# Optimization experiments

Measured on AMD Instinct MI355X. Metric: run time of the kernel, lower is better.

## Reference

```python
import jax, jax.numpy as jnp
import numpy as np

SCALE = 0.25
POOL = (7, 7)
SR = 2          # sampling_ratio
EPS = 1e-5      # LayerNorm eps
B, N, C, H, W = 4, 256, 256, 128, 128
D = 1024
IN_DIM = C * POOL[0] * POOL[1]


def _layer_norm(x, g, b):
    m = x.mean(-1, keepdims=True)
    v = ((x - m) ** 2).mean(-1, keepdims=True)
    return (x - m) / jnp.sqrt(v + EPS) * g + b


def _roi_align_one(feat, ys, xs):
    # feat [C,H,W]; ys [N,PH]; xs [N,PW] sample coords in feature-map space
    Cc, Hh, Ww = feat.shape
    y = ys[:, :, None]                      # [N,PH,1]
    x = xs[:, None, :]                      # [N,1,PW]
    valid = (y > -1.0) & (y < Hh) & (x > -1.0) & (x < Ww)  # torchvision semantics
    yc = jnp.clip(y, 0.0, Hh - 1)
    xc = jnp.clip(x, 0.0, Ww - 1)
    y0 = jnp.floor(yc).astype(jnp.int32)
    x0 = jnp.floor(xc).astype(jnp.int32)
    y1 = jnp.minimum(y0 + 1, Hh - 1)
    x1 = jnp.minimum(x0 + 1, Ww - 1)
    ly = yc - y0; lx = xc - x0
    hy = 1.0 - ly; hx = 1.0 - lx
    flat = feat.reshape(Cc, Hh * Ww)
    g = lambda yi, xi: flat[:, yi * Ww + xi]            # [C,N,PH,PW]
    val = (hy * hx) * g(y0, x0) + (hy * lx) * g(y0, x1) \
        + (ly * hx) * g(y1, x0) + (ly * lx) * g(y1, x1)
    return jnp.where(valid, val, 0.0)                    # [C,N,PH,PW]


def roi_align(feats, boxes):
    # feats [B,C,H,W]; boxes [B,N,4] in image coords -> pooled [B,N,C,ph,pw]
    Bb, Cc, Hh, Ww = feats.shape
    ph, pw = POOL
    b = boxes * SCALE
    bx1, by1, bx2, by2 = b[..., 0], b[..., 1], b[..., 2], b[..., 3]
    rw = jnp.maximum(bx2 - bx1, 1.0)
    rh = jnp.maximum(by2 - by1, 1.0)
    bh = rh / ph
    bw = rw / pw
    # sample offset k -> bin k//SR, sub-sample k%SR: (k+0.5)/SR bin-units
    oy = (jnp.arange(ph * SR, dtype=feats.dtype) + 0.5) / SR
    ox = (jnp.arange(pw * SR, dtype=feats.dtype) + 0.5) / SR
    ys = by1[..., None] + bh[..., None] * oy             # [B,N,ph*SR]
    xs = bx1[..., None] + bw[..., None] * ox             # [B,N,pw*SR]
    vals = jax.vmap(_roi_align_one)(feats, ys, xs)       # [B,C,N,PH,PW]
    Nn = boxes.shape[1]
    vals = vals.transpose(0, 2, 1, 3, 4).reshape(Bb, Nn, Cc, ph, SR, pw, SR)
    return vals.mean(axis=(4, 6))                        # avg over 2x2 samples


def setup_inputs() -> dict:
    key = jax.random.key(0)
    ks = jax.random.split(key, 8)
    feats = jax.random.normal(ks[0], (B, C, H, W), dtype=jnp.float32)
    r = jax.random.uniform(ks[1], (B, N, 4), dtype=jnp.float32)
    x1 = r[..., 0] * (512 - 64)
    y1 = r[..., 1] * (512 - 64)
    x2 = x1 + 4.0 + r[..., 2] * 60.0
    y2 = y1 + 4.0 + r[..., 3] * 60.0
    lines_box = jnp.stack([x1, y1, x2, y2], axis=-1)
    img_sizes = jnp.full((B, 2), 512, dtype=jnp.int32)
    W1 = jax.random.normal(ks[2], (IN_DIM, D), dtype=jnp.float32) / np.sqrt(IN_DIM)
    b1 = jnp.zeros((D,), jnp.float32)
    W2 = jax.random.normal(ks[3], (D, D), dtype=jnp.float32) / np.sqrt(D)
    b2 = jnp.zeros((D,), jnp.float32)
    bbox_W = jax.random.normal(ks[4], (4, D), dtype=jnp.float32) / 2.0
    bbox_b = jnp.zeros((D,), jnp.float32)
    ln_bbox_g = jnp.ones((D,), jnp.float32); ln_bbox_b = jnp.zeros((D,), jnp.float32)
    ln_add_g = jnp.ones((D,), jnp.float32); ln_add_b = jnp.zeros((D,), jnp.float32)
    return {"feats": feats, "lines_box": lines_box, "img_sizes": img_sizes,
            "W1": W1, "b1": b1, "W2": W2, "b2": b2,
            "bbox_W": bbox_W, "bbox_b": bbox_b,
            "ln_bbox_g": ln_bbox_g, "ln_bbox_b": ln_bbox_b,
            "ln_add_g": ln_add_g, "ln_add_b": ln_add_b}


def reference(feats, lines_box, img_sizes, W1, b1, W2, b2, bbox_W, bbox_b,
              ln_bbox_g, ln_bbox_b, ln_add_g, ln_add_b):
    Bb = feats.shape[0]
    Hh, Ww = feats.shape[-2:]
    Nn = lines_box.shape[1]
    pooled = roi_align(feats, lines_box).reshape(Bb, Nn, -1)   # [B,N,C*ph*pw]
    h = jax.nn.relu(pooled @ W1 + b1) @ W2 + b2                # [B,N,D]
    # per-image box normalization: x*scale/feats_W, y*scale/feats_H
    norm = SCALE * jnp.array([1.0 / Ww, 1.0 / Hh, 1.0 / Ww, 1.0 / Hh], feats.dtype)
    nb = lines_box * norm
    p = _layer_norm(nb @ bbox_W + bbox_b, ln_bbox_g, ln_bbox_b)
    return _layer_norm(h + p, ln_add_g, ln_add_b)              # [B,N,D]
```

## Files before the change

kernel.cpp:

```cpp
#include <hip/hip_runtime.h>
#include <hip/hip_bf16.h>

typedef __attribute__((ext_vector_type(8))) short short8;
typedef __attribute__((ext_vector_type(4))) float floatx4;

#define AS1(p) ((const __attribute__((address_space(1))) void*)(p))
#define AS3(p) ((__attribute__((address_space(3))) void*)(p))

__device__ __forceinline__ float bf_lo(unsigned u) { return __uint_as_float(u << 16); }
__device__ __forceinline__ float bf_hi(unsigned u) { return __uint_as_float(u & 0xffff0000u); }

__global__ __launch_bounds__(512) void prep_kernel(
    const float* __restrict__ feats, const float* __restrict__ W1, const float* __restrict__ W2,
    __hip_bfloat16* __restrict__ featsT, __hip_bfloat16* __restrict__ W1T,
    __hip_bfloat16* __restrict__ W2T)
{
    __shared__ float tile[256][68];
    const int t = threadIdx.x;
    const int w = t >> 6, l = t & 63;
    const int bid = blockIdx.x;

    const float* src;
    __hip_bfloat16* dst;
    size_t sstride, dstride;

    if (bid < 1024) {
        const int b = bid >> 8, hwt = bid & 255;
        src = feats + (size_t)b * 256 * 16384 + hwt * 64;
        sstride = 16384;
        dst = featsT + ((size_t)b * 16384 + hwt * 64) * 256;
        dstride = 256;
    } else if (bid < 1808) {
        const int r = bid - 1024;
        const int bin = r >> 4, nt = r & 15;
        src = W1 + (size_t)bin * 1024 + nt * 64;
        sstride = 49 * 1024;
        dst = W1T + (size_t)(nt * 64) * 12544 + bin * 256;
        dstride = 12544;
    } else {
        const int r = bid - 1808;
        const int kt = r >> 4, nt = r & 15;
        src = W2 + (size_t)(kt * 256) * 1024 + nt * 64;
        sstride = 1024;
        dst = W2T + (size_t)(nt * 64) * 1024 + kt * 256;
        dstride = 1024;
    }

    #pragma unroll
    for (int i = 0; i < 8; ++i) {
        const int r  = i * 32 + w * 4 + (l >> 4);
        const int c4 = (l & 15) * 4;
        const float4 v = *(const float4*)(src + (size_t)r * sstride + c4);
        *(float4*)&tile[r][c4 ^ (((r >> 3) & 15) << 2)] = v;
    }
    __syncthreads();

    #pragma unroll
    for (int i = 0; i < 4; ++i) {
        const int d  = i * 16 + w * 2 + (l >> 5);
        const int a  = l & 31;
        const int c8 = a * 8;
        const int dsw = d ^ ((a & 15) << 2);
        union { __hip_bfloat16 h[8]; uint4 u; } o;
        #pragma unroll
        for (int j = 0; j < 8; ++j)
            o.h[j] = __float2bfloat16(tile[c8 + j][dsw]);
        *(uint4*)(dst + (size_t)d * dstride + c8) = o.u;
    }
}

__global__ __launch_bounds__(256) void roi_kernel4(
    const __hip_bfloat16* __restrict__ featsT, const float* __restrict__ boxes,
    __hip_bfloat16* __restrict__ pooled)
{
    __shared__ int   sy0[14], sy1[14], sx0[14], sx1[14];
    __shared__ float sly[14], svy[14], slx[14], svx[14];
    const int tid  = threadIdx.x;
    const int bn   = blockIdx.x >> 1;
    const int half = blockIdx.x & 1;
    if (tid < 28) {
        const int  i   = tid % 14;
        const bool isx = tid >= 14;
        const float lo = boxes[bn * 4 + (isx ? 0 : 1)] * 0.25f;
        const float hi = boxes[bn * 4 + (isx ? 2 : 3)] * 0.25f;
        const float szb = fmaxf(hi - lo, 1.0f) * (1.0f / 7.0f);
        const float coord = lo + szb * ((i + 0.5f) * 0.5f);
        const float valid = (coord > -1.0f && coord < 128.0f) ? 1.0f : 0.0f;
        const float cc = fminf(fmaxf(coord, 0.0f), 127.0f);
        const int i0 = (int)floorf(cc);
        const int i1 = min(i0 + 1, 127);
        const float l = cc - (float)i0;
        if (isx) { sx0[i] = i0; sx1[i] = i1; slx[i] = l; svx[i] = valid; }
        else     { sy0[i] = i0; sy1[i] = i1; sly[i] = l; svy[i] = valid; }
    }
    __syncthreads();
    const int wave = tid >> 6;
    const int lane = tid & 63;
    const int sub  = lane >> 5;
    const int co   = lane & 31;
    const int b    = bn >> 8;
    const __hip_bfloat16* fb = featsT + (size_t)b * 4194304 + co * 8;
    __hip_bfloat16* po = pooled + (size_t)bn * 12544 + co * 8;

    const int pstart = (half ? 12 : 0) + wave;
    const int pend   = half ? 25 : 12;
    for (int p = pstart; p < pend; p += 4) {
        int bin = 2 * p + sub;
        if (bin > 48) bin = 48;
        const int ph = (bin * 37) >> 8;
        const int pw = bin - ph * 7;
        float s0 = 0.f, s1 = 0.f, s2 = 0.f, s3 = 0.f;
        float s4 = 0.f, s5 = 0.f, s6 = 0.f, s7 = 0.f;
        #pragma unroll
        for (int sy = 0; sy < 2; ++sy) {
            const int iy = ph * 2 + sy;
            const int y0 = sy0[iy], y1 = sy1[iy];
            const float ly = sly[iy], wy = svy[iy];
            const float hy = 1.f - ly;
            #pragma unroll
            for (int sx = 0; sx < 2; ++sx) {
                const int ix = pw * 2 + sx;
                const int x0 = sx0[ix], x1 = sx1[ix];
                const float lx = slx[ix], wx = svx[ix];
                const float hx = 1.f - lx;
                const uint4 u00 = *(const uint4*)(fb + (((y0 << 7) + x0) * 256));
                const uint4 u01 = *(const uint4*)(fb + (((y0 << 7) + x1) * 256));
                const uint4 u10 = *(const uint4*)(fb + (((y1 << 7) + x0) * 256));
                const uint4 u11 = *(const uint4*)(fb + (((y1 << 7) + x1) * 256));
                const float wv  = wy * wx;
                const float w00 = hy * hx * wv, w01 = hy * lx * wv;
                const float w10 = ly * hx * wv, w11 = ly * lx * wv;
                s0 += w00 * bf_lo(u00.x) + w01 * bf_lo(u01.x) + w10 * bf_lo(u10.x) + w11 * bf_lo(u11.x);
                s1 += w00 * bf_hi(u00.x) + w01 * bf_hi(u01.x) + w10 * bf_hi(u10.x) + w11 * bf_hi(u11.x);
                s2 += w00 * bf_lo(u00.y) + w01 * bf_lo(u01.y) + w10 * bf_lo(u10.y) + w11 * bf_lo(u11.y);
                s3 += w00 * bf_hi(u00.y) + w01 * bf_hi(u01.y) + w10 * bf_hi(u10.y) + w11 * bf_hi(u11.y);
                s4 += w00 * bf_lo(u00.z) + w01 * bf_lo(u01.z) + w10 * bf_lo(u10.z) + w11 * bf_lo(u11.z);
                s5 += w00 * bf_hi(u00.z) + w01 * bf_hi(u01.z) + w10 * bf_hi(u10.z) + w11 * bf_hi(u11.z);
                s6 += w00 * bf_lo(u00.w) + w01 * bf_lo(u01.w) + w10 * bf_lo(u10.w) + w11 * bf_lo(u11.w);
                s7 += w00 * bf_hi(u00.w) + w01 * bf_hi(u01.w) + w10 * bf_hi(u10.w) + w11 * bf_hi(u11.w);
            }
        }
        union { __hip_bfloat16 h[8]; uint4 u; } o;
        o.h[0] = __float2bfloat16(s0 * 0.25f);
        o.h[1] = __float2bfloat16(s1 * 0.25f);
        o.h[2] = __float2bfloat16(s2 * 0.25f);
        o.h[3] = __float2bfloat16(s3 * 0.25f);
        o.h[4] = __float2bfloat16(s4 * 0.25f);
        o.h[5] = __float2bfloat16(s5 * 0.25f);
        o.h[6] = __float2bfloat16(s6 * 0.25f);
        o.h[7] = __float2bfloat16(s7 * 0.25f);
        *(uint4*)(po + bin * 256) = o.u;
    }
}

__global__ __launch_bounds__(512, 2) void gemm1_8phase(
    const __hip_bfloat16* __restrict__ A,
    const __hip_bfloat16* __restrict__ BT,
    __hip_bfloat16* __restrict__ Cpart)
{
    constexpr int K = 12544;
    constexpr int KCHUNK = 896;
    constexpr int NKT = 14;
    constexpr int ITERS = 7;

    __shared__ char lds[131072];

    const int bid = blockIdx.x;
    const int xcd = bid & 7;
    const int sl  = bid >> 3;
    const int z   = xcd + 8 * (sl >> 4);
    if (z >= 14) return;
    const int tile = sl & 15;
    const int by = tile >> 2, bx = tile & 3;
    const int m0 = by << 8, n0 = bx << 8;
    const int k0 = z * KCHUNK;

    const int tid  = threadIdx.x;
    const int lane = tid & 63;
    const int wave = tid >> 6;
    const int wm   = wave >> 2;
    const int wn   = wave & 3;
    const int l15  = lane & 15;
    const int kq   = (lane >> 4) << 3;

    floatx4 acc[8][4] = {};
    short8 bf[4][2];

    auto stage = [&](const __hip_bfloat16* gsrc, int ldsoff) {
        #pragma unroll
        for (int j = 0; j < 2; ++j) {
            const int lin = j * 8192 + tid * 16;
            const int r   = lin >> 7;
            const int cs  = ((lin & 127) ^ ((r & 7) << 4)) >> 1;
            __builtin_amdgcn_global_load_lds(AS1(gsrc + (size_t)r * K + cs),
                                             AS3(lds + ldsoff + lin), 16, 0, 0);
        }
    };

#define PHASE(SLOT, MQ, FIRSTB, STAGE_STMT, VM)                                    \
    {                                                                               \
        if (FIRSTB) {                                                               \
            _Pragma("unroll")                                                       \
            for (int nf = 0; nf < 4; ++nf) {                                        \
                const int nl = wn * 64 + nf * 16 + l15;                             \
                const int bh = nl >> 7, br = nl & 127;                              \
                _Pragma("unroll")                                                   \
                for (int ks = 0; ks < 2; ++ks)                                      \
                    bf[nf][ks] = *(const short8*)(lds + (SLOT) * 65536 + 32768      \
                        + bh * 16384 + br * 128                                     \
                        + (((ks * 32 + kq) * 2) ^ ((br & 7) << 4)));                \
            }                                                                       \
        }                                                                           \
        short8 af[2][2];                                                            \
        _Pragma("unroll")                                                           \
        for (int mf = 0; mf < 2; ++mf) {                                            \
            const int ar = (MQ) * 32 + mf * 16 + l15;                               \
            _Pragma("unroll")                                                       \
            for (int ks = 0; ks < 2; ++ks)                                          \
                af[mf][ks] = *(const short8*)(lds + (SLOT) * 65536 + wm * 16384     \
                    + ar * 128 + (((ks * 32 + kq) * 2) ^ ((ar & 7) << 4)));         \
        }                                                                           \
        STAGE_STMT;                                                                 \
        __builtin_amdgcn_s_barrier();                                               \
        asm volatile("s_waitcnt lgkmcnt(0)" ::: "memory");                          \
        __builtin_amdgcn_s_setprio(1);                                              \
        _Pragma("unroll")                                                           \
        for (int mf = 0; mf < 2; ++mf)                                              \
            _Pragma("unroll")                                                       \
            for (int nf = 0; nf < 4; ++nf)                                          \
                _Pragma("unroll")                                                   \
                for (int ks = 0; ks < 2; ++ks)                                      \
                    acc[(MQ) * 2 + mf][nf] = __builtin_amdgcn_mfma_f32_16x16x32_bf16( \
                        af[mf][ks], bf[nf][ks], acc[(MQ) * 2 + mf][nf], 0, 0, 0);   \
        __builtin_amdgcn_s_setprio(0);                                              \
        if (VM) asm volatile("s_waitcnt vmcnt(4)" ::: "memory");                    \
        __builtin_amdgcn_s_barrier();                                               \
    }

    stage(BT + (size_t)n0 * K + k0,               32768);
    stage(BT + (size_t)(n0 + 128) * K + k0,       32768 + 16384);
    stage(A  + (size_t)m0 * K + k0,               0);
    stage(A  + (size_t)(m0 + 128) * K + k0,       16384);
    stage(BT + (size_t)n0 * K + k0 + 64,          65536 + 32768);
    stage(BT + (size_t)(n0 + 128) * K + k0 + 64,  65536 + 32768 + 16384);
    asm volatile("s_waitcnt vmcnt(4)" ::: "memory");
    __builtin_amdgcn_s_barrier();

    for (int it = 0; it < ITERS; ++it) {
        const int t1 = 2 * it + 1;
        int t2 = 2 * it + 2; if (t2 > NKT - 1) t2 = NKT - 1;
        int t3 = 2 * it + 3; if (t3 > NKT - 1) t3 = NKT - 1;
        PHASE(0, 0, true,  stage(A  + (size_t)m0 * K + k0 + t1 * 64,          65536),          0);
        PHASE(0, 1, false, stage(A  + (size_t)(m0 + 128) * K + k0 + t1 * 64,  65536 + 16384),  0);
        PHASE(0, 2, false, stage(BT + (size_t)n0 * K + k0 + t2 * 64,          32768),          0);
        PHASE(0, 3, false, stage(BT + (size_t)(n0 + 128) * K + k0 + t2 * 64,  32768 + 16384),  1);
        PHASE(1, 0, true,  stage(A  + (size_t)m0 * K + k0 + t2 * 64,          0),              0);
        PHASE(1, 1, false, stage(A  + (size_t)(m0 + 128) * K + k0 + t2 * 64,  16384),          0);
        PHASE(1, 2, false, stage(BT + (size_t)n0 * K + k0 + t3 * 64,          65536 + 32768),  0);
        PHASE(1, 3, false, stage(BT + (size_t)(n0 + 128) * K + k0 + t3 * 64,  65536 + 32768 + 16384), 1);
    }
#undef PHASE

    __hip_bfloat16* cp = Cpart + (size_t)z * (1024 * 1024) + (size_t)m0 * 1024 + n0;
    const int r4 = (lane >> 4) << 2;
    #pragma unroll
    for (int mi = 0; mi < 8; ++mi)
        #pragma unroll
        for (int nf = 0; nf < 4; ++nf)
            #pragma unroll
            for (int r = 0; r < 4; ++r)
                cp[(size_t)(wm * 128 + mi * 16 + r4 + r) * 1024 + wn * 64 + nf * 16 + l15] =
                    __float2bfloat16(acc[mi][nf][r]);
}

__global__ __launch_bounds__(256) void gemm_bf16_kernel(
    const __hip_bfloat16* __restrict__ A,
    const __hip_bfloat16* __restrict__ BT,
    __hip_bfloat16* __restrict__ Cpart,
    int Mdim, int Ndim, int K, int kChunk)
{
    __shared__ __hip_bfloat16 lsA[128 * 64];
    __shared__ __hip_bfloat16 lsB[128 * 64];
    const int tid  = threadIdx.x;
    const int lane = tid & 63;
    const int wave = tid >> 6;
    const int wrow = (wave >> 1) << 6;
    const int wcol = (wave & 1) << 6;
    const int m0 = blockIdx.y << 7;
    const int n0 = blockIdx.x << 7;
    const int k0 = blockIdx.z * kChunk;

    floatx4 acc[4][4] = {};

    const int strow = tid >> 3;
    const int scol  = ((tid & 7) ^ (strow & 7)) << 3;
    const __hip_bfloat16* aSrc = A  + (size_t)(m0 + strow) * K + k0 + scol;
    const __hip_bfloat16* bSrc = BT + (size_t)(n0 + strow) * K + k0 + scol;
    __hip_bfloat16* ldsA = lsA + tid * 8;
    __hip_bfloat16* ldsB = lsB + tid * 8;
    const size_t rowJump = (size_t)32 * K;

    const int row16 = lane & 15;
    const int kg    = (lane >> 4) << 3;
    const int nk = kChunk >> 6;
    for (int kk = 0; kk < nk; ++kk) {
        __syncthreads();
        #pragma unroll
        for (int g = 0; g < 4; ++g) {
            __builtin_amdgcn_global_load_lds(AS1(aSrc + g * rowJump), AS3(ldsA + g * 2048), 16, 0, 0);
            __builtin_amdgcn_global_load_lds(AS1(bSrc + g * rowJump), AS3(ldsB + g * 2048), 16, 0, 0);
        }
        __syncthreads();
        #pragma unroll
        for (int ks = 0; ks < 2; ++ks) {
            short8 af[4], bfr[4];
            #pragma unroll
            for (int m = 0; m < 4; ++m) {
                const int ar = wrow + m * 16 + row16;
                af[m] = *(const short8*)(lsA + ar * 64 + ((ks * 32 + kg) ^ ((ar & 7) << 3)));
            }
            #pragma unroll
            for (int n = 0; n < 4; ++n) {
                const int br = wcol + n * 16 + row16;
                bfr[n] = *(const short8*)(lsB + br * 64 + ((ks * 32 + kg) ^ ((br & 7) << 3)));
            }
            #pragma unroll
            for (int m = 0; m < 4; ++m)
                #pragma unroll
                for (int n = 0; n < 4; ++n)
                    acc[m][n] = __builtin_amdgcn_mfma_f32_16x16x32_bf16(af[m], bfr[n], acc[m][n], 0, 0, 0);
        }
        aSrc += 64; bSrc += 64;
    }
    __hip_bfloat16* cp = Cpart + (size_t)blockIdx.z * Mdim * Ndim + (size_t)m0 * Ndim + n0;
    const int r4 = (lane >> 4) << 2;
    #pragma unroll
    for (int m = 0; m < 4; ++m)
        #pragma unroll
        for (int n = 0; n < 4; ++n)
            #pragma unroll
            for (int r = 0; r < 4; ++r)
                cp[(size_t)(wrow + m * 16 + r4 + r) * Ndim + (wcol + n * 16 + row16)] =
                    __float2bfloat16(acc[m][n][r]);
}

__global__ __launch_bounds__(256) void reduce_relu_kernel(
    const __hip_bfloat16* __restrict__ part, const float* __restrict__ bias,
    __hip_bfloat16* __restrict__ out, int nsplit)
{
    const size_t MN = 1024 * 1024;
    const int idx = (blockIdx.x * 256 + threadIdx.x) * 8;
    float s[8] = {};
    for (int z = 0; z < nsplit; ++z) {
        const uint4 v = *(const uint4*)(part + z * MN + idx);
        s[0] += bf_lo(v.x); s[1] += bf_hi(v.x);
        s[2] += bf_lo(v.y); s[3] += bf_hi(v.y);
        s[4] += bf_lo(v.z); s[5] += bf_hi(v.z);
        s[6] += bf_lo(v.w); s[7] += bf_hi(v.w);
    }
    const int jb = idx & 1023;
    const floatx4 b0 = *(const floatx4*)(bias + jb);
    const floatx4 b1v = *(const floatx4*)(bias + jb + 4);
    union { __hip_bfloat16 h[8]; uint4 u; } o;
    #pragma unroll
    for (int i = 0; i < 4; ++i) {
        const float v0 = s[i] + b0[i];
        o.h[i] = __float2bfloat16(v0 > 0.0f ? v0 : 0.0f);
    }
    #pragma unroll
    for (int i = 0; i < 4; ++i) {
        const float v1 = s[4 + i] + b1v[i];
        o.h[4 + i] = __float2bfloat16(v1 > 0.0f ? v1 : 0.0f);
    }
    *(uint4*)(out + idx) = o.u;
}

__device__ inline void block_stats(float s, float ss, float* red, float& mean, float& rstd)
{
    #pragma unroll
    for (int o = 32; o > 0; o >>= 1) {
        s  += __shfl_down(s, o, 64);
        ss += __shfl_down(ss, o, 64);
    }
    const int wave = threadIdx.x >> 6;
    const int lane = threadIdx.x & 63;
    __syncthreads();
    if (lane == 0) { red[wave] = s; red[8 + wave] = ss; }
    __syncthreads();
    const float a = red[0] + red[1] + red[2] + red[3];
    const float b = red[8] + red[9] + red[10] + red[11];
    mean = a * (1.0f / 1024.0f);
    const float var = b * (1.0f / 1024.0f) - mean * mean;
    rstd = rsqrtf(var + 1e-5f);
}

__global__ __launch_bounds__(256) void final_kernel(
    const __hip_bfloat16* __restrict__ part2, const float* __restrict__ b2,
    const float* __restrict__ boxes,
    const float* __restrict__ bboxW, const float* __restrict__ bboxb,
    const float* __restrict__ g1, const float* __restrict__ bb1,
    const float* __restrict__ g2, const float* __restrict__ bb2,
    float* __restrict__ out)
{
    __shared__ float red[16];
    const int row = blockIdx.x;
    const int j0 = threadIdx.x * 4;
    const size_t MN = 1024 * 1024;

    floatx4 h = *(const floatx4*)(b2 + j0);
    #pragma unroll
    for (int z = 0; z < 4; ++z) {
        const uint2 v = *(const uint2*)(part2 + z * MN + (size_t)row * 1024 + j0);
        h[0] += bf_lo(v.x); h[1] += bf_hi(v.x);
        h[2] += bf_lo(v.y); h[3] += bf_hi(v.y);
    }

    const float sc = 0.25f / 128.0f;
    const float nb0 = boxes[row * 4 + 0] * sc;
    const float nb1 = boxes[row * 4 + 1] * sc;
    const float nb2 = boxes[row * 4 + 2] * sc;
    const float nb3 = boxes[row * 4 + 3] * sc;

    floatx4 p = *(const floatx4*)(bboxb + j0);
    p += nb0 * *(const floatx4*)(bboxW + j0);
    p += nb1 * *(const floatx4*)(bboxW + 1024 + j0);
    p += nb2 * *(const floatx4*)(bboxW + 2048 + j0);
    p += nb3 * *(const floatx4*)(bboxW + 3072 + j0);

    float mean, rstd;
    block_stats(p[0] + p[1] + p[2] + p[3],
                p[0]*p[0] + p[1]*p[1] + p[2]*p[2] + p[3]*p[3], red, mean, rstd);
    const floatx4 pg = *(const floatx4*)(g1 + j0);
    const floatx4 pb = *(const floatx4*)(bb1 + j0);
    floatx4 x;
    #pragma unroll
    for (int i = 0; i < 4; ++i)
        x[i] = h[i] + ((p[i] - mean) * rstd * pg[i] + pb[i]);

    block_stats(x[0] + x[1] + x[2] + x[3],
                x[0]*x[0] + x[1]*x[1] + x[2]*x[2] + x[3]*x[3], red, mean, rstd);
    const floatx4 og = *(const floatx4*)(g2 + j0);
    const floatx4 ob = *(const floatx4*)(bb2 + j0);
    floatx4 o;
    #pragma unroll
    for (int i = 0; i < 4; ++i)
        o[i] = (x[i] - mean) * rstd * og[i] + ob[i];
    *(floatx4*)(out + (size_t)row * 1024 + j0) = o;
}

extern "C" void kernel_launch(void* const* d_in, const int* in_sizes, int n_in,
                              void* d_out, int out_size, void* d_ws, size_t ws_size,
                              hipStream_t stream)
{
    const float* feats = (const float*)d_in[0];
    const float* boxes = (const float*)d_in[1];
    const float* W1    = (const float*)d_in[3];
    const float* b1    = (const float*)d_in[4];
    const float* W2    = (const float*)d_in[5];
    const float* b2    = (const float*)d_in[6];
    const float* bboxW = (const float*)d_in[7];
    const float* bboxb = (const float*)d_in[8];
    const float* g1    = (const float*)d_in[9];
    const float* bb1   = (const float*)d_in[10];
    const float* g2    = (const float*)d_in[11];
    const float* bb2   = (const float*)d_in[12];
    float* out = (float*)d_out;

    char* ws = (char*)d_ws;
    __hip_bfloat16* W1T    = (__hip_bfloat16*)(ws);
    __hip_bfloat16* W2T    = (__hip_bfloat16*)(ws + 25690112);
    __hip_bfloat16* pooled = (__hip_bfloat16*)(ws + 27787264);
    __hip_bfloat16* part1  = (__hip_bfloat16*)(ws + 53477376);
    __hip_bfloat16* part2  = part1;
    __hip_bfloat16* featsT = (__hip_bfloat16*)(ws + 53477376);
    __hip_bfloat16* A2     = (__hip_bfloat16*)(ws + 87031808);

    prep_kernel<<<1872, 512, 0, stream>>>(feats, W1, W2, featsT, W1T, W2T);
    roi_kernel4<<<2048, 256, 0, stream>>>(featsT, boxes, pooled);
    gemm1_8phase<<<256, 512, 0, stream>>>(pooled, W1T, part1);
    reduce_relu_kernel<<<512, 256, 0, stream>>>(part1, b1, A2, 14);
    gemm_bf16_kernel<<<dim3(8, 8, 4), 256, 0, stream>>>(A2, W2T, part2, 1024, 1024, 1024, 256);
    final_kernel<<<1024, 256, 0, stream>>>(part2, b2, boxes, bboxW, bboxb, g1, bb1, g2, bb2, out);
}
```

Before: 108.1 us.

## Overlap weight transposes with ROI pooling in one interleaved kernel

The single prep kernel is split in two. Feature transposition stays in its own launch. The W1/W2 transpose-to-bf16 tiles are interleaved block-wise with ROI-align blocks in a new fused kernel, so weight conversion overlaps the gather-heavy pooling. Tiles become 64x128 with a padded LDS array instead of XOR swizzling, and each ROI block now covers all bins with 512 threads instead of two half-blocks. This adds a branchy block scheduler and a larger shared-memory footprint for the ROI blocks, which may reduce occupancy.

Measured after the change: 105.4 us. 2.5% less time.

```diff
diff --git a/kernel.cpp b/kernel.cpp
--- a/kernel.cpp
+++ b/kernel.cpp
@@ -10,74 +10,85 @@
 __device__ __forceinline__ float bf_lo(unsigned u) { return __uint_as_float(u << 16); }
 __device__ __forceinline__ float bf_hi(unsigned u) { return __uint_as_float(u & 0xffff0000u); }
 
-__global__ __launch_bounds__(512) void prep_kernel(
-    const float* __restrict__ feats, const float* __restrict__ W1, const float* __restrict__ W2,
-    __hip_bfloat16* __restrict__ featsT, __hip_bfloat16* __restrict__ W1T,
-    __hip_bfloat16* __restrict__ W2T)
-{
-    __shared__ float tile[256][68];
-    const int t = threadIdx.x;
-    const int w = t >> 6, l = t & 63;
+__device__ __forceinline__ void transpose_tile_64x128(
+    const float* __restrict__ src, __hip_bfloat16* __restrict__ dst,
+    size_t sstride, size_t dstride, float (*tile)[129], int t)
+{
+    #pragma unroll
+    for (int i = 0; i < 4; ++i) {
+        const int r  = i * 16 + (t >> 5);
+        const int c4 = (t & 31) * 4;
+        const float4 v = *(const float4*)(src + (size_t)r * sstride + c4);
+        *(float4*)&tile[r][c4] = v;
+    }
+    __syncthreads();
+    #pragma unroll
+    for (int i = 0; i < 2; ++i) {
+        const int d  = i * 64 + (t >> 3);
+        const int c8 = (t & 7) * 8;
+        union { __hip_bfloat16 h[8]; uint4 u; } o;
+        #pragma unroll
+        for (int j = 0; j < 8; ++j)
+            o.h[j] = __float2bfloat16(tile[c8 + j][d]);
+        *(uint4*)(dst + (size_t)d * dstride + c8) = o.u;
+    }
+}
+
+__global__ __launch_bounds__(512) void prep_feats_kernel(
+    const float* __restrict__ feats, __hip_bfloat16* __restrict__ featsT)
+{
+    __shared__ float tile[64][129];
     const int bid = blockIdx.x;
-
-    const float* src;
-    __hip_bfloat16* dst;
-    size_t sstride, dstride;
-
-    if (bid < 1024) {
-        const int b = bid >> 8, hwt = bid & 255;
-        src = feats + (size_t)b * 256 * 16384 + hwt * 64;
-        sstride = 16384;
-        dst = featsT + ((size_t)b * 16384 + hwt * 64) * 256;
-        dstride = 256;
-    } else if (bid < 1808) {
-        const int r = bid - 1024;
-        const int bin = r >> 4, nt = r & 15;
-        src = W1 + (size_t)bin * 1024 + nt * 64;
-        sstride = 49 * 1024;
-        dst = W1T + (size_t)(nt * 64) * 12544 + bin * 256;
-        dstride = 12544;
-    } else {
-        const int r = bid - 1808;
-        const int kt = r >> 4, nt = r & 15;
-        src = W2 + (size_t)(kt * 256) * 1024 + nt * 64;
-        sstride = 1024;
-        dst = W2T + (size_t)(nt * 64) * 1024 + kt * 256;
-        dstride = 1024;
-    }
-
-    #pragma unroll
-    for (int i = 0; i < 8; ++i) {
-        const int r  = i * 32 + w * 4 + (l >> 4);
-        const int c4 = (l & 15) * 4;
-        const float4 v = *(const float4*)(src + (size_t)r * sstride + c4);
-        *(float4*)&tile[r][c4 ^ (((r >> 3) & 15) << 2)] = v;
-    }
-    __syncthreads();
-
-    #pragma unroll
-    for (int i = 0; i < 4; ++i) {
-        const int d  = i * 16 + w * 2 + (l >> 5);
-        const int a  = l & 31;
-        const int c8 = a * 8;
-        const int dsw = d ^ ((a & 15) << 2);
-        union { __hip_bfloat16 h[8]; uint4 u; } o;
-        #pragma unroll
-        for (int j = 0; j < 8; ++j)
-            o.h[j] = __float2bfloat16(tile[c8 + j][dsw]);
-        *(uint4*)(dst + (size_t)d * dstride + c8) = o.u;
-    }
-}
-
-__global__ __launch_bounds__(256) void roi_kernel4(
+    const int b   = bid >> 9;
+    const int rem = bid & 511;
+    const int ct  = rem >> 7;
+    const int hwt = rem & 127;
+    const float* src = feats + (size_t)(b * 256 + ct * 64) * 16384 + hwt * 128;
+    __hip_bfloat16* dst = featsT + ((size_t)b * 16384 + hwt * 128) * 256 + ct * 64;
+    transpose_tile_64x128(src, dst, 16384, 256, tile, threadIdx.x);
+}
+
+__global__ __launch_bounds__(512) void roi_fused_kernel(
     const __hip_bfloat16* __restrict__ featsT, const float* __restrict__ boxes,
-    __hip_bfloat16* __restrict__ pooled)
-{
+    __hip_bfloat16* __restrict__ pooled,
+    const float* __restrict__ W1, const float* __restrict__ W2,
+    __hip_bfloat16* __restrict__ W1T, __hip_bfloat16* __restrict__ W2T)
+{
+    __shared__ float tile[64][129];
     __shared__ int   sy0[14], sy1[14], sx0[14], sx1[14];
     __shared__ float sly[14], svy[14], slx[14], svx[14];
-    const int tid  = threadIdx.x;
-    const int bn   = blockIdx.x >> 1;
-    const int half = blockIdx.x & 1;
+    const int tid = threadIdx.x;
+    const int bid = blockIdx.x;
+    const int rp  = (bid * 32) / 85;
+    const int rn  = ((bid + 1) * 32) / 85;
+
+    if (rn == rp) {
+        int t_idx = bid - rp;
+        const float* src;
+        __hip_bfloat16* dst;
+        size_t sstride, dstride;
+        if (t_idx < 1568) {
+            const int bin = t_idx >> 5;
+            const int rem = t_idx & 31;
+            const int ct  = rem >> 3;
+            const int nt  = rem & 7;
+            src = W1  + ((size_t)(ct * 64) * 49 + bin) * 1024 + nt * 128;
+            sstride = 49 * 1024;
+            dst = W1T + (size_t)(nt * 128) * 12544 + bin * 256 + ct * 64;
+            dstride = 12544;
+        } else {
+            const int u  = t_idx - 1568;
+            const int kt = u >> 3, nt = u & 7;
+            src = W2  + (size_t)(kt * 64) * 1024 + nt * 128;
+            sstride = 1024;
+            dst = W2T + (size_t)(nt * 128) * 1024 + kt * 64;
+            dstride = 1024;
+        }
+        transpose_tile_64x128(src, dst, sstride, dstride, tile, tid);
+        return;
+    }
+
+    const int bn = rp;
     if (tid < 28) {
         const int  i   = tid % 14;
         const bool isx = tid >= 14;
@@ -102,9 +113,7 @@
     const __hip_bfloat16* fb = featsT + (size_t)b * 4194304 + co * 8;
     __hip_bfloat16* po = pooled + (size_t)bn * 12544 + co * 8;
 
-    const int pstart = (half ? 12 : 0) + wave;
-    const int pend   = half ? 25 : 12;
-    for (int p = pstart; p < pend; p += 4) {
+    for (int p = wave; p < 25; p += 8) {
         int bin = 2 * p + sub;
         if (bin > 48) bin = 48;
         const int ph = (bin * 37) >> 8;
@@ -475,8 +484,8 @@
     __hip_bfloat16* featsT = (__hip_bfloat16*)(ws + 53477376);
     __hip_bfloat16* A2     = (__hip_bfloat16*)(ws + 87031808);
 
-    prep_kernel<<<1872, 512, 0, stream>>>(feats, W1, W2, featsT, W1T, W2T);
-    roi_kernel4<<<2048, 256, 0, stream>>>(featsT, boxes, pooled);
+    prep_feats_kernel<<<2048, 512, 0, stream>>>(feats, featsT);
+    roi_fused_kernel<<<2720, 512, 0, stream>>>(featsT, boxes, pooled, W1, W2, W1T, W2T);
     gemm1_8phase<<<256, 512, 0, stream>>>(pooled, W1T, part1);
     reduce_relu_kernel<<<512, 256, 0, stream>>>(part1, b1, A2, 14);
     gemm_bf16_kernel<<<dim3(8, 8, 4), 256, 0, stream>>>(A2, W2T, part2, 1024, 1024, 1024, 256);
```
